# Kernel optimization log

Hardware: AMD Instinct MI355X
Metric: run time of the kernel (lower is better)

Reference implementation:

```python
import jax, jax.numpy as jnp
import numpy as np

B, K, D, C = 16384, 8, 128, 128


def setup_inputs() -> dict:
    key = jax.random.key(0)
    k1, k2, k3, k4, k5 = jax.random.split(key, 5)
    return {
        "graph_embeddings": jax.random.normal(k1, (B, D), dtype=jnp.float32),
        "retrieval_embeddings": jax.random.normal(k2, (B, K, D), dtype=jnp.float32),
        "W_adapter": jax.random.normal(k3, (D, D), dtype=jnp.float32) / np.sqrt(D),
        "W_pred": jax.random.normal(k4, (D, C), dtype=jnp.float32) / np.sqrt(D),
        "b_pred": jnp.zeros((C,), dtype=jnp.float32),
        "labels": jax.random.randint(k5, (B, K), 0, C, dtype=jnp.int64).astype(jnp.int32),
    }


def reference(graph_embeddings, retrieval_embeddings, W_adapter, W_pred, b_pred, labels):
    # g_label = Softmax(dim=1)(graph_pred_linear(graph_embeddings))   [B, C]
    g_label = jax.nn.softmax(graph_embeddings @ W_pred + b_pred, axis=1)

    # concat_H = cat([graph_embeddings] + retrievals, -1).view(B, K+1, D)
    concat_H = jnp.concatenate([graph_embeddings[:, None, :], retrieval_embeddings], axis=1)  # [B, K+1, D]

    # adapter: bilinear attention scores, softmax over the K+1 candidates
    scores = jnp.einsum("bd,de,bme->bm", graph_embeddings, W_adapter, concat_H)  # [B, K+1]
    attention = jax.nn.softmax(scores, axis=1)

    # generic-dataset branch of the per-sample loop, vectorized:
    #   adjusted[b] = attn[b,0] * g_label[b]
    #   adjusted[b, labels[b,k]] += attn[b, k]   for k in range(K)
    # (note: faithful to the original, which indexes attention[b][k], not k+1)
    one_hot = jax.nn.one_hot(labels, C, dtype=g_label.dtype)  # [B, K, C]
    adjusted_label = attention[:, :1] * g_label + jnp.einsum("bk,bkc->bc", attention[:, :K], one_hot)
    return adjusted_label
```

## Files before the change

### kernel.cpp

```cpp
#include <hip/hip_runtime.h>


#define SB      16
#define THREADS 256

typedef __attribute__((ext_vector_type(8))) short bfrag_t;
typedef __attribute__((ext_vector_type(4))) float facc_t;

__device__ __forceinline__ unsigned short bf16_hi_trunc(float f) {
    return (unsigned short)(__builtin_bit_cast(unsigned int, f) >> 16);
}
__device__ __forceinline__ float bf16_up(unsigned short h) {
    return __builtin_bit_cast(float, ((unsigned int)h) << 16);
}

__global__ __launch_bounds__(256)
void pack_w_kernel(const float* __restrict__ Wa, const float* __restrict__ Wp,
                   unsigned short* __restrict__ w_hi, unsigned short* __restrict__ w_lo) {
    const int t    = blockIdx.x * 256 + threadIdx.x;
    const int nt   = t >> 8;
    const int kk   = (t >> 6) & 3;
    const int lane = t & 63;
    const int n    = nt * 16 + (lane & 15);
    const int kb   = kk * 32 + (lane >> 4) * 8;
    const float* W = (n < 128) ? Wa : Wp;
    const int col  = n & 127;
    unsigned int h[4], l[4];
    #pragma unroll
    for (int i = 0; i < 4; ++i) {
        const float v0 = W[(kb + 2 * i) * 128 + col];
        const float v1 = W[(kb + 2 * i + 1) * 128 + col];
        const unsigned short h0 = bf16_hi_trunc(v0), h1 = bf16_hi_trunc(v1);
        const unsigned short l0 = bf16_hi_trunc(v0 - bf16_up(h0));
        const unsigned short l1 = bf16_hi_trunc(v1 - bf16_up(h1));
        h[i] = (unsigned int)h0 | ((unsigned int)h1 << 16);
        l[i] = (unsigned int)l0 | ((unsigned int)l1 << 16);
    }
    ((uint4*)w_hi)[t] = make_uint4(h[0], h[1], h[2], h[3]);
    ((uint4*)w_lo)[t] = make_uint4(l[0], l[1], l[2], l[3]);
}

__global__ __launch_bounds__(THREADS, 4)
void graph_retrieval_fused(const float* __restrict__ G,
                           const float* __restrict__ R,
                           const unsigned short* __restrict__ w_hi,
                           const unsigned short* __restrict__ w_lo,
                           const float* __restrict__ bp,
                           const int*   __restrict__ labels,
                           float* __restrict__ out)
{
    __shared__ float g_lds[SB * 132];
    __shared__ float t_lds[SB * 132];
    __shared__ float logit_lds[SB * 132];
    __shared__ float attn_lds[SB * 8];
    __shared__ float stat_m[SB], stat_iz[SB];
    __shared__ int   lab_lds[SB * 8];

    const int tid  = threadIdx.x;
    const int b0   = blockIdx.x * SB;
    const int wv   = tid >> 6;
    const int lane = tid & 63;

    {
        const float4* Gv = (const float4*)(G + (size_t)b0 * 128);
        #pragma unroll
        for (int rpt = 0; rpt < 2; ++rpt) {
            const int idx = rpt * 256 + tid;
            const int row = idx >> 5, j = idx & 31;
            ((float4*)g_lds)[row * 33 + j] = Gv[idx];
        }
        if (tid < SB * 8) lab_lds[tid] = labels[b0 * 8 + tid];
    }
    __syncthreads();

    {
        const int arow = lane & 15;
        const int kch  = lane >> 4;
        bfrag_t a_hi[4], a_lo[4];
        #pragma unroll
        for (int kk = 0; kk < 4; ++kk) {
            const float* src = &g_lds[arow * 132 + kk * 32 + kch * 8];
            const float4 f0 = *(const float4*)src;
            const float4 f1 = *(const float4*)(src + 4);
            const float f[8] = {f0.x, f0.y, f0.z, f0.w, f1.x, f1.y, f1.z, f1.w};
            #pragma unroll
            for (int i = 0; i < 8; ++i) {
                const unsigned short hb = bf16_hi_trunc(f[i]);
                a_hi[kk][i] = (short)hb;
                a_lo[kk][i] = (short)bf16_hi_trunc(f[i] - bf16_up(hb));
            }
        }

        facc_t acc[4] = {{0.f,0.f,0.f,0.f},{0.f,0.f,0.f,0.f},
                         {0.f,0.f,0.f,0.f},{0.f,0.f,0.f,0.f}};
        #pragma unroll
        for (int p = 0; p < 4; ++p) {
            const int nt = wv * 4 + p;
            #pragma unroll
            for (int kk = 0; kk < 4; ++kk) {
                const int idx = (nt * 4 + kk) * 64 + lane;
                const bfrag_t bh = ((const bfrag_t*)w_hi)[idx];
                const bfrag_t bl = ((const bfrag_t*)w_lo)[idx];
                acc[p] = __builtin_amdgcn_mfma_f32_16x16x32_bf16(a_hi[kk], bh, acc[p], 0, 0, 0);
                acc[p] = __builtin_amdgcn_mfma_f32_16x16x32_bf16(a_lo[kk], bh, acc[p], 0, 0, 0);
                acc[p] = __builtin_amdgcn_mfma_f32_16x16x32_bf16(a_hi[kk], bl, acc[p], 0, 0, 0);
            }
        }

        const int crow = (lane >> 4) * 4;
        #pragma unroll
        for (int p = 0; p < 4; ++p) {
            const int coll = p * 16 + (lane & 15);
            if (wv < 2) {
                const int c_t = wv * 64 + coll;
                #pragma unroll
                for (int j = 0; j < 4; ++j)
                    t_lds[(crow + j) * 132 + c_t] = acc[p][j];
            } else {
                const int c_l = (wv - 2) * 64 + coll;
                const float bias = bp[c_l];
                #pragma unroll
                for (int j = 0; j < 4; ++j)
                    logit_lds[(crow + j) * 132 + c_l] = acc[p][j] + bias;
            }
        }
    }
    __syncthreads();

    {
        const int s0 = wv * 4;

        float mx[4], zs[4];
        float2 ev[4];
        #pragma unroll
        for (int q = 0; q < 4; ++q) {
            ev[q] = *(const float2*)&logit_lds[(s0 + q) * 132 + 2 * lane];
            mx[q] = fmaxf(ev[q].x, ev[q].y);
        }
        #pragma unroll
        for (int off = 32; off > 0; off >>= 1)
            #pragma unroll
            for (int q = 0; q < 4; ++q)
                mx[q] = fmaxf(mx[q], __shfl_xor(mx[q], off, 64));
        #pragma unroll
        for (int q = 0; q < 4; ++q)
            zs[q] = __expf(ev[q].x - mx[q]) + __expf(ev[q].y - mx[q]);
        #pragma unroll
        for (int off = 32; off > 0; off >>= 1)
            #pragma unroll
            for (int q = 0; q < 4; ++q)
                zs[q] += __shfl_xor(zs[q], off, 64);
        if (lane == 0) {
            #pragma unroll
            for (int q = 0; q < 4; ++q) {
                stat_m[s0 + q]  = mx[q];
                stat_iz[s0 + q] = 1.f / zs[q];
            }
        }

        float sc[4][9];
        #pragma unroll
        for (int q = 0; q < 4; ++q) {
            const int s = s0 + q;
            const float2 t2 = *(const float2*)&t_lds[s * 132 + 2 * lane];
            const float2 g2 = *(const float2*)&g_lds[s * 132 + 2 * lane];
            sc[q][0] = t2.x * g2.x + t2.y * g2.y;
            const float2* Rr = (const float2*)(R + (size_t)(b0 + s) * 1024);
            #pragma unroll
            for (int m = 1; m < 9; ++m) {
                const float2 r2 = Rr[(m - 1) * 64 + lane];
                sc[q][m] = t2.x * r2.x + t2.y * r2.y;
            }
        }
        #pragma unroll
        for (int off = 32; off > 0; off >>= 1)
            #pragma unroll
            for (int q = 0; q < 4; ++q)
                #pragma unroll
                for (int m = 0; m < 9; ++m)
                    sc[q][m] += __shfl_xor(sc[q][m], off, 64);

        #pragma unroll
        for (int q = 0; q < 4; ++q) {
            float m9 = sc[q][0];
            #pragma unroll
            for (int m = 1; m < 9; ++m) m9 = fmaxf(m9, sc[q][m]);
            float e[9], sum = 0.f;
            #pragma unroll
            for (int m = 0; m < 9; ++m) { e[m] = __expf(sc[q][m] - m9); sum += e[m]; }
            const float inv = 1.f / sum;
            if (lane == 0) {
                #pragma unroll
                for (int m = 0; m < 8; ++m)
                    attn_lds[(s0 + q) * 8 + m] = e[m] * inv;
            }
        }
    }
    __syncthreads();

    {
        const int c  = tid & 127;
        const int hh = tid >> 7;
        #pragma unroll
        for (int i = 0; i < 8; ++i) {
            const int s = hh * 8 + i;
            const float lg = logit_lds[s * 132 + c];
            const float gl = __expf(lg - stat_m[s]) * stat_iz[s];
            const int4   la = *(const int4*)&lab_lds[s * 8];
            const int4   lb = *(const int4*)&lab_lds[s * 8 + 4];
            const float4 a0 = *(const float4*)&attn_lds[s * 8];
            const float4 a1 = *(const float4*)&attn_lds[s * 8 + 4];
            float val = a0.x * gl;
            val += (la.x == c) ? a0.x : 0.f;
            val += (la.y == c) ? a0.y : 0.f;
            val += (la.z == c) ? a0.z : 0.f;
            val += (la.w == c) ? a0.w : 0.f;
            val += (lb.x == c) ? a1.x : 0.f;
            val += (lb.y == c) ? a1.y : 0.f;
            val += (lb.z == c) ? a1.z : 0.f;
            val += (lb.w == c) ? a1.w : 0.f;
            out[(size_t)(b0 + s) * 128 + c] = val;
        }
    }
}

extern "C" void kernel_launch(void* const* d_in, const int* in_sizes, int n_in,
                              void* d_out, int out_size, void* d_ws, size_t ws_size,
                              hipStream_t stream) {
    const float* G      = (const float*)d_in[0];
    const float* R      = (const float*)d_in[1];
    const float* Wa     = (const float*)d_in[2];
    const float* Wp     = (const float*)d_in[3];
    const float* bpred  = (const float*)d_in[4];
    const int*   labels = (const int*)d_in[5];
    float*       o      = (float*)d_out;

    unsigned short* w_hi = (unsigned short*)d_ws;
    unsigned short* w_lo = w_hi + 4096 * 8;

    hipLaunchKernelGGL(pack_w_kernel, dim3(16), dim3(256), 0, stream,
                       Wa, Wp, w_hi, w_lo);

    const int B = in_sizes[0] / 128;
    hipLaunchKernelGGL(graph_retrieval_fused, dim3(B / SB), dim3(THREADS), 0, stream,
                       G, R, w_hi, w_lo, bpred, labels, o);
}
```

Measured before the change: 120.1 us.

## Double block threads and rework score dot-products into 8-lane float4 groups

After: 116.6 us. -2.9%, faster.

```diff
diff --git a/kernel.cpp b/kernel.cpp
--- a/kernel.cpp
+++ b/kernel.cpp
@@ -2,7 +2,7 @@
 
 
 #define SB      16
-#define THREADS 256
+#define THREADS 512
 
 typedef __attribute__((ext_vector_type(8))) short bfrag_t;
 typedef __attribute__((ext_vector_type(4))) float facc_t;
@@ -12,6 +12,9 @@
 }
 __device__ __forceinline__ float bf16_up(unsigned short h) {
     return __builtin_bit_cast(float, ((unsigned int)h) << 16);
+}
+__device__ __forceinline__ float dot4(float4 a, float4 b) {
+    return a.x * b.x + a.y * b.y + a.z * b.z + a.w * b.w;
 }
 
 __global__ __launch_bounds__(256)
@@ -60,15 +63,12 @@
     const int b0   = blockIdx.x * SB;
     const int wv   = tid >> 6;
     const int lane = tid & 63;
+    const int s0   = wv * 2;
 
     {
         const float4* Gv = (const float4*)(G + (size_t)b0 * 128);
-        #pragma unroll
-        for (int rpt = 0; rpt < 2; ++rpt) {
-            const int idx = rpt * 256 + tid;
-            const int row = idx >> 5, j = idx & 31;
-            ((float4*)g_lds)[row * 33 + j] = Gv[idx];
-        }
+        const int row = tid >> 5, jj = tid & 31;
+        ((float4*)g_lds)[row * 33 + jj] = Gv[tid];
         if (tid < SB * 8) lab_lds[tid] = labels[b0 * 8 + tid];
     }
     __syncthreads();
@@ -91,11 +91,10 @@
             }
         }
 
-        facc_t acc[4] = {{0.f,0.f,0.f,0.f},{0.f,0.f,0.f,0.f},
-                         {0.f,0.f,0.f,0.f},{0.f,0.f,0.f,0.f}};
-        #pragma unroll
-        for (int p = 0; p < 4; ++p) {
-            const int nt = wv * 4 + p;
+        facc_t acc[2] = {{0.f,0.f,0.f,0.f},{0.f,0.f,0.f,0.f}};
+        #pragma unroll
+        for (int p = 0; p < 2; ++p) {
+            const int nt = wv * 2 + p;
             #pragma unroll
             for (int kk = 0; kk < 4; ++kk) {
                 const int idx = (nt * 4 + kk) * 64 + lane;
@@ -108,16 +107,17 @@
         }
 
         const int crow = (lane >> 4) * 4;
-        #pragma unroll
-        for (int p = 0; p < 4; ++p) {
-            const int coll = p * 16 + (lane & 15);
-            if (wv < 2) {
-                const int c_t = wv * 64 + coll;
+        const int coll = lane & 15;
+        #pragma unroll
+        for (int p = 0; p < 2; ++p) {
+            const int nt = wv * 2 + p;
+            if (nt < 8) {
+                const int c_t = nt * 16 + coll;
                 #pragma unroll
                 for (int j = 0; j < 4; ++j)
                     t_lds[(crow + j) * 132 + c_t] = acc[p][j];
             } else {
-                const int c_l = (wv - 2) * 64 + coll;
+                const int c_l = (nt - 8) * 16 + coll;
                 const float bias = bp[c_l];
                 #pragma unroll
                 for (int j = 0; j < 4; ++j)
@@ -128,71 +128,82 @@
     __syncthreads();
 
     {
-        const int s0 = wv * 4;
-
-        float mx[4], zs[4];
-        float2 ev[4];
-        #pragma unroll
-        for (int q = 0; q < 4; ++q) {
+        float mx[2], zs[2];
+        float2 ev[2];
+        #pragma unroll
+        for (int q = 0; q < 2; ++q) {
             ev[q] = *(const float2*)&logit_lds[(s0 + q) * 132 + 2 * lane];
             mx[q] = fmaxf(ev[q].x, ev[q].y);
         }
         #pragma unroll
         for (int off = 32; off > 0; off >>= 1)
             #pragma unroll
-            for (int q = 0; q < 4; ++q)
+            for (int q = 0; q < 2; ++q)
                 mx[q] = fmaxf(mx[q], __shfl_xor(mx[q], off, 64));
         #pragma unroll
-        for (int q = 0; q < 4; ++q)
+        for (int q = 0; q < 2; ++q)
             zs[q] = __expf(ev[q].x - mx[q]) + __expf(ev[q].y - mx[q]);
         #pragma unroll
         for (int off = 32; off > 0; off >>= 1)
             #pragma unroll
-            for (int q = 0; q < 4; ++q)
+            for (int q = 0; q < 2; ++q)
                 zs[q] += __shfl_xor(zs[q], off, 64);
         if (lane == 0) {
             #pragma unroll
-            for (int q = 0; q < 4; ++q) {
+            for (int q = 0; q < 2; ++q) {
                 stat_m[s0 + q]  = mx[q];
                 stat_iz[s0 + q] = 1.f / zs[q];
             }
         }
-
-        float sc[4][9];
-        #pragma unroll
-        for (int q = 0; q < 4; ++q) {
+    }
+
+    {
+        const int gg = lane >> 3, jj2 = lane & 7;
+        float sc0[2], scm[2];
+        #pragma unroll
+        for (int q = 0; q < 2; ++q) {
             const int s = s0 + q;
-            const float2 t2 = *(const float2*)&t_lds[s * 132 + 2 * lane];
-            const float2 g2 = *(const float2*)&g_lds[s * 132 + 2 * lane];
-            sc[q][0] = t2.x * g2.x + t2.y * g2.y;
-            const float2* Rr = (const float2*)(R + (size_t)(b0 + s) * 1024);
-            #pragma unroll
-            for (int m = 1; m < 9; ++m) {
-                const float2 r2 = Rr[(m - 1) * 64 + lane];
-                sc[q][m] = t2.x * r2.x + t2.y * r2.y;
-            }
-        }
-        #pragma unroll
-        for (int off = 32; off > 0; off >>= 1)
-            #pragma unroll
-            for (int q = 0; q < 4; ++q)
-                #pragma unroll
-                for (int m = 0; m < 9; ++m)
-                    sc[q][m] += __shfl_xor(sc[q][m], off, 64);
-
-        #pragma unroll
-        for (int q = 0; q < 4; ++q) {
-            float m9 = sc[q][0];
-            #pragma unroll
-            for (int m = 1; m < 9; ++m) m9 = fmaxf(m9, sc[q][m]);
+            const float* tb = &t_lds[s * 132 + jj2 * 16];
+            const float* gb = &g_lds[s * 132 + jj2 * 16];
+            const float* rb = R + (size_t)(b0 + s) * 1024 + gg * 128 + jj2 * 16;
+            float p0 = 0.f, pm = 0.f;
+            #pragma unroll
+            for (int e = 0; e < 4; ++e) {
+                const float4 tv = *(const float4*)(tb + e * 4);
+                const float4 gv = *(const float4*)(gb + e * 4);
+                const float4 rv = *(const float4*)(rb + e * 4);
+                p0 += dot4(tv, gv);
+                pm += dot4(tv, rv);
+            }
+            sc0[q] = p0; scm[q] = pm;
+        }
+        #pragma unroll
+        for (int off = 1; off < 8; off <<= 1) {
+            #pragma unroll
+            for (int q = 0; q < 2; ++q) {
+                sc0[q] += __shfl_xor(sc0[q], off, 64);
+                scm[q] += __shfl_xor(scm[q], off, 64);
+            }
+        }
+        #pragma unroll
+        for (int q = 0; q < 2; ++q) {
+            const int s = s0 + q;
+            float sc9[9];
+            sc9[0] = sc0[q];
+            #pragma unroll
+            for (int m = 1; m < 9; ++m)
+                sc9[m] = __shfl(scm[q], (m - 1) * 8, 64);
+            float m9 = sc9[0];
+            #pragma unroll
+            for (int m = 1; m < 9; ++m) m9 = fmaxf(m9, sc9[m]);
             float e[9], sum = 0.f;
             #pragma unroll
-            for (int m = 0; m < 9; ++m) { e[m] = __expf(sc[q][m] - m9); sum += e[m]; }
+            for (int m = 0; m < 9; ++m) { e[m] = __expf(sc9[m] - m9); sum += e[m]; }
             const float inv = 1.f / sum;
             if (lane == 0) {
                 #pragma unroll
                 for (int m = 0; m < 8; ++m)
-                    attn_lds[(s0 + q) * 8 + m] = e[m] * inv;
+                    attn_lds[s * 8 + m] = e[m] * inv;
             }
         }
     }
@@ -202,8 +213,8 @@
         const int c  = tid & 127;
         const int hh = tid >> 7;
         #pragma unroll
-        for (int i = 0; i < 8; ++i) {
-            const int s = hh * 8 + i;
+        for (int i = 0; i < 4; ++i) {
+            const int s = hh * 4 + i;
             const float lg = logit_lds[s * 132 + c];
             const float gl = __expf(lg - stat_m[s]) * stat_iz[s];
             const int4   la = *(const int4*)&lab_lds[s * 8];
```
